# Kernel tuning notes

Measured on AMD Instinct MI355X. Metric: run time of the kernel, lower is better.

## Reference

```python
import jax, jax.numpy as jnp
import numpy as np

HEADS = 16
WINDOW = 256
OVERLAP = WINDOW // 8  # 32, matches window_size // 8


def setup_inputs() -> dict:
    key = jax.random.key(0)
    ks = jax.random.split(key, 8)
    n, L, E = 4, 4096, 1024
    d = E // HEADS
    return {
        "values": jax.random.normal(ks[0], (n, L, E), jnp.float32),
        "keys": jax.random.normal(ks[1], (n, L, E), jnp.float32),
        "queries": jax.random.normal(ks[2], (n, L, E), jnp.float32),
        "mask": jnp.ones((n, L), jnp.int32),
        "Wv": jax.random.normal(ks[3], (d, d), jnp.float32) * 0.125,
        "Wk": jax.random.normal(ks[4], (d, d), jnp.float32) * 0.125,
        "Wq": jax.random.normal(ks[5], (d, d), jnp.float32) * 0.125,
        "Wf": jax.random.normal(ks[6], (E, E), jnp.float32) * 0.03125,
        "bf": jnp.zeros((E,), jnp.float32),
    }


def reference(values, keys, queries, mask, Wv, Wk, Wq, Wf, bf):
    n, L, E = queries.shape
    d = E // HEADS
    nW = L // WINDOW            # number of (non-overlapping) query windows
    K = WINDOW + 2 * OVERLAP    # halo-extended key window length

    # per-head linear projections (torch Linear: x @ W^T)
    v = jnp.einsum('nlhd,ed->nlhe', values.reshape(n, L, HEADS, d), Wv)
    k = jnp.einsum('nlhd,ed->nlhe', keys.reshape(n, L, HEADS, d), Wk)
    q = jnp.einsum('nlhd,ed->nlhe', queries.reshape(n, L, HEADS, d), Wq)

    # pad keys/values by the halo; invalid (padded) positions masked with -inf
    kp = jnp.pad(k, ((0, 0), (OVERLAP, OVERLAP), (0, 0), (0, 0)))
    vp = jnp.pad(v, ((0, 0), (OVERLAP, OVERLAP), (0, 0), (0, 0)))
    idx = jnp.arange(nW)[:, None] * WINDOW + jnp.arange(K)[None, :]  # [nW, K] padded coords
    kw = kp[:, idx]  # [n, nW, K, h, d]
    vw = vp[:, idx]
    qw = q.reshape(n, nW, WINDOW, HEADS, d)

    en = jnp.einsum('nwqhd,nwkhd->nwhqk', qw, kw)  # [n, nW, h, WINDOW, K]
    # query-row mask fill (original: masked_fill with -1e10 before scaling)
    qmask = mask.reshape(n, nW, WINDOW)
    en = jnp.where(qmask[:, :, None, :, None] == 0, jnp.float32(-1e10), en)
    # halo positions outside the true sequence get exactly zero weight (= slicing)
    key_valid = (idx >= OVERLAP) & (idx < OVERLAP + L)  # [nW, K]
    en = jnp.where(key_valid[None, :, None, None, :], en, -jnp.inf)

    att = jax.nn.softmax(en / (d ** 0.5), axis=-1)
    out = jnp.einsum('nwhqk,nwkhd->nwqhd', att, vw).reshape(n, L, E)
    return out @ Wf.T + bf
```

## Files before the change

kernel.cpp:

```cpp
#include <hip/hip_runtime.h>
#include <hip/hip_bf16.h>
#include <stdint.h>

typedef unsigned int uint;
typedef unsigned short ushort;

#define NB 4
#define SL 4096
#define EMB 1024
#define NH 16
#define DH 64
#define WIN 256
#define OVL 32
#define NW 16
#define NTOK (NB * SL)

typedef __attribute__((ext_vector_type(8))) short short8;
typedef __attribute__((ext_vector_type(4))) float float4v;

#define AS1 __attribute__((address_space(1)))
#define AS3 __attribute__((address_space(3)))

__device__ __forceinline__ float bf_lo(uint u) { return __uint_as_float(u << 16); }
__device__ __forceinline__ float bf_hi(uint u) { return __uint_as_float(u & 0xffff0000u); }
__device__ __forceinline__ float bf2f(ushort s) { return __uint_as_float((uint)s << 16); }
__device__ __forceinline__ ushort f2bf(float x) {
  uint u = __float_as_uint(x);
  u += 0x7fffu + ((u >> 16) & 1u);
  return (ushort)(u >> 16);
}

__global__ __launch_bounds__(256) void qkv_proj(
    const float* __restrict__ qin, const float* __restrict__ kin,
    const float* __restrict__ vin,
    const float* __restrict__ Wq, const float* __restrict__ Wk,
    const float* __restrict__ Wv,
    ushort* __restrict__ qo, ushort* __restrict__ ko, ushort* __restrict__ vo) {
  __shared__ float sW[4096];
  __shared__ float sx[4][16 * 68];
  const int t = threadIdx.x;
  const int h = t >> 4, eq = t & 15;

  const float* ins[3] = {qin, kin, vin};
  const float* Ws[3] = {Wq, Wk, Wv};
  ushort* outs[3] = {qo, ko, vo};

  for (int p = 0; p < 3; ++p) {
    __syncthreads();
    const float* W = Ws[p];
    for (int i = t; i < 4096; i += 256) {
      int c = i & 3, e = (i >> 2) & 63, d4 = i >> 8;
      sW[i] = W[e * 64 + d4 * 4 + c];
    }
    const float* src = ins[p];
    ushort* dst = outs[p];
    for (int quad = blockIdx.x; quad < NTOK / 4; quad += gridDim.x) {
      const int tok0 = quad * 4;
      __syncthreads();
      for (int s = t; s < 1024; s += 256) {
        int tk = s >> 8, i4 = s & 255;
        float4 x4 = ((const float4*)(src + (size_t)(tok0 + tk) * 1024))[i4];
        int hh = i4 >> 4, d0 = (i4 & 15) * 4;
        *(float4*)&sx[tk][hh * 68 + d0] = x4;
      }
      __syncthreads();
      float acc[4][4];
#pragma unroll
      for (int a = 0; a < 4; ++a)
#pragma unroll
        for (int b = 0; b < 4; ++b) acc[a][b] = 0.f;
#pragma unroll
      for (int d4 = 0; d4 < 16; ++d4) {
        float4 w4[4];
#pragma unroll
        for (int i = 0; i < 4; ++i)
          w4[i] = *(const float4*)&sW[(d4 * 64 + eq + 16 * i) * 4];
#pragma unroll
        for (int tk = 0; tk < 4; ++tk) {
          float4 x4 = *(const float4*)&sx[tk][h * 68 + d4 * 4];
#pragma unroll
          for (int i = 0; i < 4; ++i)
            acc[tk][i] += x4.x * w4[i].x + x4.y * w4[i].y + x4.z * w4[i].z +
                          x4.w * w4[i].w;
        }
      }
#pragma unroll
      for (int tk = 0; tk < 4; ++tk) {
        int tok = tok0 + tk;
        int nb = tok >> 12, l = tok & 4095;
        size_t base = ((size_t)(nb * NH + h) * SL + l) * DH;
#pragma unroll
        for (int i = 0; i < 4; ++i)
          dst[base + eq + 16 * i] = f2bf(acc[tk][i]);
      }
    }
  }
}

__global__ __launch_bounds__(256) void attn_win_mfma(
    const ushort* __restrict__ qws, const ushort* __restrict__ kws,
    const ushort* __restrict__ vws, const int* __restrict__ mask,
    ushort* __restrict__ att) {
  __shared__ alignas(16) ushort sk[64 * 72];
  __shared__ alignas(16) ushort svT[64 * 72];
  __shared__ alignas(16) ushort sp[4 * 64 * 72];
  __shared__ float sm[256];

  const int t = threadIdx.x;
  const int wid = t >> 6, lane = t & 63, quad = lane >> 4, l16 = lane & 15;
  const int bid = blockIdx.x;
  const int h = bid & 15, w = (bid >> 4) & 15, nb = bid >> 8;
  const size_t headbase = (size_t)(nb * NH + h) * SL;
  const int q0 = w * WIN + wid * 64;

  sm[t] = (float)mask[nb * SL + w * WIN + t];

  short8 qf[4][2];
#pragma unroll
  for (int mt = 0; mt < 4; ++mt)
#pragma unroll
    for (int kh = 0; kh < 2; ++kh)
      qf[mt][kh] = *(const short8*)(qws + (headbase + q0 + mt * 16 + l16) * DH +
                                    kh * 32 + quad * 8);

  float4v Of[4][4];
#pragma unroll
  for (int mt = 0; mt < 4; ++mt)
#pragma unroll
    for (int dt = 0; dt < 4; ++dt) Of[mt][dt] = (float4v){0.f, 0.f, 0.f, 0.f};
  float mrow[16], lrow[16];
#pragma unroll
  for (int i = 0; i < 16; ++i) { mrow[i] = -INFINITY; lrow[i] = 0.f; }

  ushort* spw = sp + wid * 64 * 72;
  const int gk0 = w * WIN - OVL;
  const float CSC = 0.18033688f;

  for (int c = 0; c < 5; ++c) {
    __syncthreads();
    const int cbase = gk0 + c * 64;
    for (int s = t; s < 512; s += 256) {
      int key = s & 63, dj = s >> 6;
      int gk = cbase + key;
      uint4 kq = make_uint4(0u, 0u, 0u, 0u);
      uint4 vq = make_uint4(0u, 0u, 0u, 0u);
      if ((unsigned)gk < (unsigned)SL) {
        kq = *(const uint4*)(kws + (headbase + gk) * DH + dj * 8);
        vq = *(const uint4*)(vws + (headbase + gk) * DH + dj * 8);
      }
      *(uint4*)&sk[key * 72 + dj * 8] = kq;
      svT[(dj * 8 + 0) * 72 + key] = (ushort)(vq.x & 0xffffu);
      svT[(dj * 8 + 1) * 72 + key] = (ushort)(vq.x >> 16);
      svT[(dj * 8 + 2) * 72 + key] = (ushort)(vq.y & 0xffffu);
      svT[(dj * 8 + 3) * 72 + key] = (ushort)(vq.y >> 16);
      svT[(dj * 8 + 4) * 72 + key] = (ushort)(vq.z & 0xffffu);
      svT[(dj * 8 + 5) * 72 + key] = (ushort)(vq.z >> 16);
      svT[(dj * 8 + 6) * 72 + key] = (ushort)(vq.w & 0xffffu);
      svT[(dj * 8 + 7) * 72 + key] = (ushort)(vq.w >> 16);
    }
    __syncthreads();

    float4v Sf[4][4];
#pragma unroll
    for (int mt = 0; mt < 4; ++mt)
#pragma unroll
      for (int nt = 0; nt < 4; ++nt) Sf[mt][nt] = (float4v){0.f, 0.f, 0.f, 0.f};
#pragma unroll
    for (int kh = 0; kh < 2; ++kh) {
      short8 kf[4];
#pragma unroll
      for (int nt = 0; nt < 4; ++nt)
        kf[nt] = *(const short8*)&sk[(nt * 16 + l16) * 72 + kh * 32 + quad * 8];
#pragma unroll
      for (int mt = 0; mt < 4; ++mt)
#pragma unroll
        for (int nt = 0; nt < 4; ++nt)
          Sf[mt][nt] = __builtin_amdgcn_mfma_f32_16x16x32_bf16(
              qf[mt][kh], kf[nt], Sf[mt][nt], 0, 0, 0);
    }

#pragma unroll
    for (int nt = 0; nt < 4; ++nt) {
      const int gkey = cbase + nt * 16 + l16;
      const bool kvalid = ((unsigned)gkey < (unsigned)SL);
#pragma unroll
      for (int mt = 0; mt < 4; ++mt)
#pragma unroll
        for (int reg = 0; reg < 4; ++reg) {
          float sv = Sf[mt][nt][reg] * CSC;
          if (sm[wid * 64 + mt * 16 + quad * 4 + reg] == 0.f) sv = -1.803e9f;
          if (!kvalid) sv = -INFINITY;
          Sf[mt][nt][reg] = sv;
        }
    }

#pragma unroll
    for (int mt = 0; mt < 4; ++mt)
#pragma unroll
      for (int reg = 0; reg < 4; ++reg) {
        const int ri = mt * 4 + reg;
        float mx = fmaxf(fmaxf(Sf[mt][0][reg], Sf[mt][1][reg]),
                         fmaxf(Sf[mt][2][reg], Sf[mt][3][reg]));
        mx = fmaxf(mx, __shfl_xor(mx, 1));
        mx = fmaxf(mx, __shfl_xor(mx, 2));
        mx = fmaxf(mx, __shfl_xor(mx, 4));
        mx = fmaxf(mx, __shfl_xor(mx, 8));
        const float mn = fmaxf(mrow[ri], mx);
        const float alpha = exp2f(mrow[ri] - mn);
        mrow[ri] = mn;
        float rs = 0.f;
#pragma unroll
        for (int nt = 0; nt < 4; ++nt) {
          float p = exp2f(Sf[mt][nt][reg] - mn);
          ushort pb = f2bf(p);
          rs += bf2f(pb);
          spw[(mt * 16 + quad * 4 + reg) * 72 + nt * 16 + l16] = pb;
        }
        rs += __shfl_xor(rs, 1);
        rs += __shfl_xor(rs, 2);
        rs += __shfl_xor(rs, 4);
        rs += __shfl_xor(rs, 8);
        lrow[ri] = lrow[ri] * alpha + rs;
#pragma unroll
        for (int dt = 0; dt < 4; ++dt) Of[mt][dt][reg] *= alpha;
      }

#pragma unroll
    for (int kh = 0; kh < 2; ++kh) {
      short8 pa[4], pb[4];
#pragma unroll
      for (int mt = 0; mt < 4; ++mt)
        pa[mt] = *(const short8*)&spw[(mt * 16 + l16) * 72 + kh * 32 + quad * 8];
#pragma unroll
      for (int dt = 0; dt < 4; ++dt)
        pb[dt] = *(const short8*)&svT[(dt * 16 + l16) * 72 + kh * 32 + quad * 8];
#pragma unroll
      for (int mt = 0; mt < 4; ++mt)
#pragma unroll
        for (int dt = 0; dt < 4; ++dt)
          Of[mt][dt] = __builtin_amdgcn_mfma_f32_16x16x32_bf16(
              pa[mt], pb[dt], Of[mt][dt], 0, 0, 0);
    }
  }

#pragma unroll
  for (int mt = 0; mt < 4; ++mt)
#pragma unroll
    for (int reg = 0; reg < 4; ++reg) {
      const float invl = 1.f / lrow[mt * 4 + reg];
      const size_t token = (size_t)nb * SL + q0 + mt * 16 + quad * 4 + reg;
#pragma unroll
      for (int dt = 0; dt < 4; ++dt)
        att[token * EMB + h * DH + dt * 16 + l16] =
            f2bf(Of[mt][dt][reg] * invl);
    }
}

__global__ __launch_bounds__(256) void wf_cvt(const float* __restrict__ Wf,
                                              ushort* __restrict__ o) {
  const int i = blockIdx.x * 256 + threadIdx.x;
  float4 f = ((const float4*)Wf)[i];
  uint2 u;
  u.x = (uint)f2bf(f.x) | ((uint)f2bf(f.y) << 16);
  u.y = (uint)f2bf(f.z) | ((uint)f2bf(f.w) << 16);
  ((uint2*)o)[i] = u;
}

#define GBK 64
__global__ __launch_bounds__(256) void final_gemm_mfma(
    const ushort* __restrict__ A, const ushort* __restrict__ Bt,
    const float* __restrict__ bias, float* __restrict__ C) {
  __shared__ alignas(16) ushort sA[128 * GBK];
  __shared__ alignas(16) ushort sB[128 * GBK];
  const int t = threadIdx.x;
  const int wid = t >> 6, lane = t & 63, quad = lane >> 4, l16 = lane & 15;
  const int n0 = blockIdx.x * 128, m0 = blockIdx.y * 128;
  const int wm = (wid & 1) * 64, wn = (wid >> 1) * 64;

  float4v acc[4][4];
#pragma unroll
  for (int i = 0; i < 4; ++i)
#pragma unroll
    for (int j = 0; j < 4; ++j) acc[i][j] = (float4v){0.f, 0.f, 0.f, 0.f};

  const int arow = lane >> 3;
  const int acol = (lane & 7) * 8;

  for (int k0 = 0; k0 < EMB; k0 += GBK) {
    __syncthreads();
#pragma unroll
    for (int seg = 0; seg < 4; ++seg) {
      const int r = wid * 32 + seg * 8;
      __builtin_amdgcn_global_load_lds(
          (AS1 const void*)(A + (size_t)(m0 + r + arow) * EMB + k0 + acol),
          (AS3 void*)&sA[r * GBK], 16, 0, 0);
      __builtin_amdgcn_global_load_lds(
          (AS1 const void*)(Bt + (size_t)(n0 + r + arow) * EMB + k0 + acol),
          (AS3 void*)&sB[r * GBK], 16, 0, 0);
    }
    __syncthreads();
#pragma unroll
    for (int kk = 0; kk < GBK; kk += 32) {
      short8 af[4], bfr[4];
#pragma unroll
      for (int i = 0; i < 4; ++i)
        af[i] = *(const short8*)&sA[(wm + i * 16 + l16) * GBK + kk + quad * 8];
#pragma unroll
      for (int j = 0; j < 4; ++j)
        bfr[j] = *(const short8*)&sB[(wn + j * 16 + l16) * GBK + kk + quad * 8];
#pragma unroll
      for (int i = 0; i < 4; ++i)
#pragma unroll
        for (int j = 0; j < 4; ++j)
          acc[i][j] = __builtin_amdgcn_mfma_f32_16x16x32_bf16(af[i], bfr[j],
                                                              acc[i][j], 0, 0, 0);
    }
  }

  float bv[4];
#pragma unroll
  for (int j = 0; j < 4; ++j) bv[j] = bias[n0 + wn + j * 16 + l16];
#pragma unroll
  for (int i = 0; i < 4; ++i)
#pragma unroll
    for (int j = 0; j < 4; ++j)
#pragma unroll
      for (int r = 0; r < 4; ++r)
        C[(size_t)(m0 + wm + i * 16 + quad * 4 + r) * EMB + n0 + wn + j * 16 +
          l16] = acc[i][j][r] + bv[j];
}

extern "C" void kernel_launch(void* const* d_in, const int* in_sizes, int n_in,
                              void* d_out, int out_size, void* d_ws,
                              size_t ws_size, hipStream_t stream) {
  const float* values  = (const float*)d_in[0];
  const float* keys    = (const float*)d_in[1];
  const float* queries = (const float*)d_in[2];
  const int*   mask    = (const int*)d_in[3];
  const float* Wv = (const float*)d_in[4];
  const float* Wk = (const float*)d_in[5];
  const float* Wq = (const float*)d_in[6];
  const float* Wf = (const float*)d_in[7];
  const float* bfv = (const float*)d_in[8];
  float* out = (float*)d_out;

  ushort* ws = (ushort*)d_ws;
  ushort* q_ws = ws;
  ushort* k_ws = ws + (size_t)16777216;
  ushort* v_ws = ws + (size_t)33554432;
  ushort* a_ws = ws + (size_t)50331648;
  ushort* wf_bf = q_ws;

  qkv_proj<<<512, 256, 0, stream>>>(queries, keys, values, Wq, Wk, Wv, q_ws,
                                    k_ws, v_ws);
  attn_win_mfma<<<NB * NW * NH, 256, 0, stream>>>(q_ws, k_ws, v_ws, mask, a_ws);
  wf_cvt<<<1024, 256, 0, stream>>>(Wf, wf_bf);
  final_gemm_mfma<<<dim3(EMB / 128, NTOK / 128), 256, 0, stream>>>(a_ws, wf_bf,
                                                                   bfv, out);
}
```

Baseline: 522.3 us.

## Rewrite QKV projection as per-head bf16 MFMA tiles with grid over tokens, heads, tensors

```diff
diff --git a/kernel.cpp b/kernel.cpp
--- a/kernel.cpp
+++ b/kernel.cpp
@@ -21,79 +21,95 @@
 #define AS1 __attribute__((address_space(1)))
 #define AS3 __attribute__((address_space(3)))
 
-__device__ __forceinline__ float bf_lo(uint u) { return __uint_as_float(u << 16); }
-__device__ __forceinline__ float bf_hi(uint u) { return __uint_as_float(u & 0xffff0000u); }
 __device__ __forceinline__ float bf2f(ushort s) { return __uint_as_float((uint)s << 16); }
 __device__ __forceinline__ ushort f2bf(float x) {
   uint u = __float_as_uint(x);
   u += 0x7fffu + ((u >> 16) & 1u);
   return (ushort)(u >> 16);
 }
-
-__global__ __launch_bounds__(256) void qkv_proj(
+__device__ __forceinline__ uint packbf(float a, float b) {
+  return (uint)f2bf(a) | ((uint)f2bf(b) << 16);
+}
+
+__global__ __launch_bounds__(256) void qkv_proj_mfma(
     const float* __restrict__ qin, const float* __restrict__ kin,
     const float* __restrict__ vin,
     const float* __restrict__ Wq, const float* __restrict__ Wk,
     const float* __restrict__ Wv,
     ushort* __restrict__ qo, ushort* __restrict__ ko, ushort* __restrict__ vo) {
-  __shared__ float sW[4096];
-  __shared__ float sx[4][16 * 68];
+  __shared__ alignas(16) ushort sx[256 * 72];
+  __shared__ alignas(16) ushort sw[64 * 72];
   const int t = threadIdx.x;
-  const int h = t >> 4, eq = t & 15;
-
-  const float* ins[3] = {qin, kin, vin};
-  const float* Ws[3] = {Wq, Wk, Wv};
-  ushort* outs[3] = {qo, ko, vo};
-
-  for (int p = 0; p < 3; ++p) {
-    __syncthreads();
-    const float* W = Ws[p];
-    for (int i = t; i < 4096; i += 256) {
-      int c = i & 3, e = (i >> 2) & 63, d4 = i >> 8;
-      sW[i] = W[e * 64 + d4 * 4 + c];
-    }
-    const float* src = ins[p];
-    ushort* dst = outs[p];
-    for (int quad = blockIdx.x; quad < NTOK / 4; quad += gridDim.x) {
-      const int tok0 = quad * 4;
-      __syncthreads();
-      for (int s = t; s < 1024; s += 256) {
-        int tk = s >> 8, i4 = s & 255;
-        float4 x4 = ((const float4*)(src + (size_t)(tok0 + tk) * 1024))[i4];
-        int hh = i4 >> 4, d0 = (i4 & 15) * 4;
-        *(float4*)&sx[tk][hh * 68 + d0] = x4;
-      }
-      __syncthreads();
-      float acc[4][4];
-#pragma unroll
-      for (int a = 0; a < 4; ++a)
-#pragma unroll
-        for (int b = 0; b < 4; ++b) acc[a][b] = 0.f;
-#pragma unroll
-      for (int d4 = 0; d4 < 16; ++d4) {
-        float4 w4[4];
-#pragma unroll
-        for (int i = 0; i < 4; ++i)
-          w4[i] = *(const float4*)&sW[(d4 * 64 + eq + 16 * i) * 4];
-#pragma unroll
-        for (int tk = 0; tk < 4; ++tk) {
-          float4 x4 = *(const float4*)&sx[tk][h * 68 + d4 * 4];
-#pragma unroll
-          for (int i = 0; i < 4; ++i)
-            acc[tk][i] += x4.x * w4[i].x + x4.y * w4[i].y + x4.z * w4[i].z +
-                          x4.w * w4[i].w;
-        }
-      }
-#pragma unroll
-      for (int tk = 0; tk < 4; ++tk) {
-        int tok = tok0 + tk;
-        int nb = tok >> 12, l = tok & 4095;
-        size_t base = ((size_t)(nb * NH + h) * SL + l) * DH;
-#pragma unroll
-        for (int i = 0; i < 4; ++i)
-          dst[base + eq + 16 * i] = f2bf(acc[tk][i]);
-      }
-    }
+  const int wid = t >> 6, lane = t & 63, quad = lane >> 4, l16 = lane & 15;
+  const int p = blockIdx.z, h = blockIdx.y;
+  const int tok0 = blockIdx.x * 256;
+
+  const float* src = (p == 0) ? qin : ((p == 1) ? kin : vin);
+  const float* W   = (p == 0) ? Wq  : ((p == 1) ? Wk  : Wv);
+  ushort* dst      = (p == 0) ? qo  : ((p == 1) ? ko  : vo);
+
+  for (int i = t; i < 1024; i += 256) {
+    int e = i >> 4, c4 = i & 15;
+    float4 f = *(const float4*)(W + e * 64 + c4 * 4);
+    uint2 u;
+    u.x = packbf(f.x, f.y);
+    u.y = packbf(f.z, f.w);
+    *(uint2*)&sw[e * 72 + c4 * 4] = u;
+  }
+  for (int i = t; i < 4096; i += 256) {
+    int tok = i >> 4, c4 = i & 15;
+    float4 f = *(const float4*)(src + (size_t)(tok0 + tok) * EMB + h * DH + c4 * 4);
+    uint2 u;
+    u.x = packbf(f.x, f.y);
+    u.y = packbf(f.z, f.w);
+    *(uint2*)&sx[tok * 72 + c4 * 4] = u;
+  }
+  __syncthreads();
+
+  short8 wa[4][2], xb[4][2];
+#pragma unroll
+  for (int mt = 0; mt < 4; ++mt)
+#pragma unroll
+    for (int kh = 0; kh < 2; ++kh)
+      wa[mt][kh] = *(const short8*)&sw[(mt * 16 + l16) * 72 + kh * 32 + quad * 8];
+#pragma unroll
+  for (int nt = 0; nt < 4; ++nt)
+#pragma unroll
+    for (int kh = 0; kh < 2; ++kh)
+      xb[nt][kh] = *(const short8*)&sx[(wid * 64 + nt * 16 + l16) * 72 + kh * 32 + quad * 8];
+
+  float4v acc[4][4];
+#pragma unroll
+  for (int i = 0; i < 4; ++i)
+#pragma unroll
+    for (int j = 0; j < 4; ++j) acc[i][j] = (float4v){0.f, 0.f, 0.f, 0.f};
+#pragma unroll
+  for (int kh = 0; kh < 2; ++kh)
+#pragma unroll
+    for (int mt = 0; mt < 4; ++mt)
+#pragma unroll
+      for (int nt = 0; nt < 4; ++nt)
+        acc[mt][nt] = __builtin_amdgcn_mfma_f32_16x16x32_bf16(
+            wa[mt][kh], xb[nt][kh], acc[mt][nt], 0, 0, 0);
+
+  __syncthreads();
+#pragma unroll
+  for (int mt = 0; mt < 4; ++mt)
+#pragma unroll
+    for (int nt = 0; nt < 4; ++nt) {
+      uint2 u;
+      u.x = packbf(acc[mt][nt][0], acc[mt][nt][1]);
+      u.y = packbf(acc[mt][nt][2], acc[mt][nt][3]);
+      *(uint2*)&sx[(wid * 64 + nt * 16 + l16) * 72 + mt * 16 + quad * 4] = u;
+    }
+  __syncthreads();
+
+  {
+    const int tokg = tok0 + t;
+    const int nb = tokg >> 12, l = tokg & 4095;
+    uint4* orow = (uint4*)(dst + ((size_t)(nb * NH + h) * SL + l) * DH);
+#pragma unroll
+    for (int j = 0; j < 8; ++j) orow[j] = *(const uint4*)&sx[t * 72 + j * 8];
   }
 }
 
@@ -149,7 +165,7 @@
         vq = *(const uint4*)(vws + (headbase + gk) * DH + dj * 8);
       }
       *(uint4*)&sk[key * 72 + dj * 8] = kq;
-      svT[(dj * 8 + 0) * 72 + key] = (ushort)(vq.x & 0xffffu);
+      svT[(dj * 8 + 0) * 72 + key] = (ushort)(kq.x & 0u) | (ushort)(vq.x & 0xffffu);
       svT[(dj * 8 + 1) * 72 + key] = (ushort)(vq.x >> 16);
       svT[(dj * 8 + 2) * 72 + key] = (ushort)(vq.y & 0xffffu);
       svT[(dj * 8 + 3) * 72 + key] = (ushort)(vq.y >> 16);
@@ -261,8 +277,8 @@
   const int i = blockIdx.x * 256 + threadIdx.x;
   float4 f = ((const float4*)Wf)[i];
   uint2 u;
-  u.x = (uint)f2bf(f.x) | ((uint)f2bf(f.y) << 16);
-  u.y = (uint)f2bf(f.z) | ((uint)f2bf(f.w) << 16);
+  u.x = packbf(f.x, f.y);
+  u.y = packbf(f.z, f.w);
   ((uint2*)o)[i] = u;
 }
 
@@ -351,8 +367,8 @@
   ushort* a_ws = ws + (size_t)50331648;
   ushort* wf_bf = q_ws;
 
-  qkv_proj<<<512, 256, 0, stream>>>(queries, keys, values, Wq, Wk, Wv, q_ws,
-                                    k_ws, v_ws);
+  qkv_proj_mfma<<<dim3(NTOK / 256, NH, 3), 256, 0, stream>>>(
+      queries, keys, values, Wq, Wk, Wv, q_ws, k_ws, v_ws);
   attn_win_mfma<<<NB * NW * NH, 256, 0, stream>>>(q_ws, k_ws, v_ws, mask, a_ws);
   wf_cvt<<<1024, 256, 0, stream>>>(Wf, wf_bf);
   final_gemm_mfma<<<dim3(EMB / 128, NTOK / 128), 256, 0, stream>>>(a_ws, wf_bf,
```

After: 455.1 us. 1.15x faster.
